# Performance work log

Hardware: AMD Instinct MI355X
Metric: run time of the kernel (lower is better)

The kernel has to match this reference:

```python
import jax, jax.numpy as jnp
import numpy as np

HEAD_NUM = 16

def setup_inputs() -> dict:
    key = jax.random.key(0)
    kq, kk, kv = jax.random.split(key, 3)
    shape = (4, 2048, 1024)  # [B, N, C]
    return {
        "query_layer": jax.random.normal(kq, shape, dtype=jnp.float32),
        "key_layer": jax.random.normal(kk, shape, dtype=jnp.float32),
        "value_layer": jax.random.normal(kv, shape, dtype=jnp.float32),
    }

def _split_heads(x, h):
    B, N, C = x.shape
    return x.reshape(B, N, h, C // h).transpose(0, 2, 1, 3)  # [B,H,N,d]

def reference(query_layer, key_layer, value_layer):
    B, N, C = query_layer.shape
    h = HEAD_NUM
    d = C // h
    q = _split_heads(query_layer, h)
    k = _split_heads(key_layer, h)
    v = _split_heads(value_layer, h)
    scores = jnp.einsum('bhnd,bhmd->bhnm', q, k) / jnp.sqrt(jnp.asarray(d, q.dtype))
    probs = jax.nn.softmax(scores, axis=-1)
    ctx = jnp.einsum('bhnm,bhmd->bhnd', probs, v)
    return ctx.transpose(0, 2, 1, 3).reshape(B, N, C)
```

## Files before the change

### kernel.cpp

```cpp
#include <hip/hip_runtime.h>
#include <hip/hip_bf16.h>

#define B_   4
#define N_   2048
#define C_   1024
#define NT   32
#define QSCALE 0.18033688011112042f

typedef __attribute__((ext_vector_type(8)))  short short8;
typedef __attribute__((ext_vector_type(4)))  float f32x4;
typedef __attribute__((ext_vector_type(16))) float f32x16;
typedef __attribute__((ext_vector_type(2)))  int   int2v;

__device__ __forceinline__ unsigned short f2bf(float x) {
    union { __hip_bfloat16 h; unsigned short u; } c;
    c.h = __float2bfloat16(x);
    return c.u;
}
__device__ __forceinline__ float fast_exp2(float x) {
    float r; asm("v_exp_f32 %0, %1" : "=v"(r) : "v"(x)); return r;
}
__device__ __forceinline__ int cvtpk(float a, float b) {
    int r; asm("v_cvt_pk_bf16_f32 %0, %1, %2" : "=v"(r) : "v"(a), "v"(b)); return r;
}

__global__ __launch_bounds__(256) void prepack(
    const float* __restrict__ K, const float* __restrict__ V,
    unsigned short* __restrict__ Kt, unsigned short* __restrict__ Vt)
{
    __shared__ __align__(16) unsigned short kl[4096];
    __shared__ __align__(16) unsigned short vl[4096];
    const int L = blockIdx.x;
    const int xcd = L & 7;
    const int j = L >> 3;
    const int head = xcd + 8 * (j >> 5);
    const int t = j & 31;
    const int b = head >> 4, h = head & 15;
    const int tid = threadIdx.x;
    const int r = tid >> 2, cb = tid & 3;
    const size_t head_off = (size_t)b * N_ * C_ + (size_t)h * 64;
    const int kv0 = t * 64;
    const int blk_out = head * NT + t;

    {
        const float* src = K + head_off + (size_t)(kv0 + r) * C_ + cb * 16;
        f32x4 x0 = *(const f32x4*)(src);
        f32x4 x1 = *(const f32x4*)(src + 4);
        f32x4 x2 = *(const f32x4*)(src + 8);
        f32x4 x3 = *(const f32x4*)(src + 12);
        short8 p0, p1;
        #pragma unroll
        for (int i = 0; i < 4; ++i) {
            p0[i] = (short)f2bf(x0[i]); p0[i + 4] = (short)f2bf(x1[i]);
            p1[i] = (short)f2bf(x2[i]); p1[i + 4] = (short)f2bf(x3[i]);
        }
        const int swz = (r & 7) << 3;
        *(short8*)&kl[r * 64 + ((cb * 16) ^ swz)]     = p0;
        *(short8*)&kl[r * 64 + ((cb * 16 + 8) ^ swz)] = p1;
    }
    {
        const float* src = V + head_off + (size_t)(kv0 + r) * C_ + cb * 16;
        f32x4 y0 = *(const f32x4*)(src);
        f32x4 y1 = *(const f32x4*)(src + 4);
        f32x4 y2 = *(const f32x4*)(src + 8);
        f32x4 y3 = *(const f32x4*)(src + 12);
        #pragma unroll
        for (int i = 0; i < 4; ++i) {
            int d0 = cb * 16 + i;
            vl[d0 * 64 + (r ^ ((d0 & 7) << 3))] = f2bf(y0[i]);
            int d1 = cb * 16 + 4 + i;
            vl[d1 * 64 + (r ^ ((d1 & 7) << 3))] = f2bf(y1[i]);
            int d2 = cb * 16 + 8 + i;
            vl[d2 * 64 + (r ^ ((d2 & 7) << 3))] = f2bf(y2[i]);
            int d3 = cb * 16 + 12 + i;
            vl[d3 * 64 + (r ^ ((d3 & 7) << 3))] = f2bf(y3[i]);
        }
    }
    __syncthreads();
    #pragma unroll
    for (int cc = 0; cc < 2; ++cc) {
        const int c  = tid + cc * 256;
        const int f  = c >> 6;
        const int ln = c & 63;
        const int row = (f & 1) * 32 + (ln & 31);
        const int col = (f >> 1) * 16 + (ln >> 5) * 8;
        const int sw  = (row & 7) << 3;
        short8 kk = *(const short8*)&kl[row * 64 + (col ^ sw)];
        short8 vv = *(const short8*)&vl[row * 64 + (col ^ sw)];
        *(short8*)&Kt[(size_t)blk_out * 4096 + c * 8] = kk;
        *(short8*)&Vt[(size_t)blk_out * 4096 + c * 8] = vv;
    }
}

#define MFMA32(A, B, C) __builtin_amdgcn_mfma_f32_32x32x16_bf16((A), (B), (C), 0, 0, 0)

#define TILE_BODY(T, PO0, PO1, PO2, PO3, PI0, PI1, PI2, PI3, FIRST)            \
{                                                                              \
    asm volatile("s_waitcnt vmcnt(0)" ::: "memory");                           \
    __syncthreads();                                                           \
    if ((T) + 1 < NT) stageK((T) + 1, cur ^ 1);                                \
    const unsigned short* kl = &klds[cur][0];                                  \
    f32x16 s0, s1;                                                             \
    {                                                                          \
        const float nm = (FIRST) ? 0.0f : -m_r;   \
        _Pragma("unroll")                                                      \
        for (int r = 0; r < 16; ++r) { s0[r] = nm; s1[r] = nm; }               \
    }                                                                          \
    __builtin_amdgcn_s_setprio(1);                                             \
    {                                                                          \
        short8 kf0 = *(const short8*)&kl[0 * 1024 + lofs];                     \
        short8 kf1 = *(const short8*)&kl[0 * 1024 + 512 + lofs];               \
        s0 = MFMA32(kf0, qfrag[0], s0);                                        \
        s1 = MFMA32(kf1, qfrag[0], s1);                                        \
        kf0 = *(const short8*)&kl[1 * 1024 + lofs];                            \
        kf1 = *(const short8*)&kl[1 * 1024 + 512 + lofs];                      \
        s0 = MFMA32(kf0, qfrag[1], s0);                                        \
        s1 = MFMA32(kf1, qfrag[1], s1);                                        \
        kf0 = *(const short8*)&kl[2 * 1024 + lofs];                            \
        kf1 = *(const short8*)&kl[2 * 1024 + 512 + lofs];                      \
        s0 = MFMA32(kf0, qfrag[2], s0);                                        \
        s1 = MFMA32(kf1, qfrag[2], s1);                                        \
        kf0 = *(const short8*)&kl[3 * 1024 + lofs];                            \
        kf1 = *(const short8*)&kl[3 * 1024 + 512 + lofs];                      \
        s0 = MFMA32(kf0, qfrag[3], s0);                                        \
        s1 = MFMA32(kf1, qfrag[3], s1);                                        \
    }                                                                          \
    if (!(FIRST)) {      \
        o0 = MFMA32(vr0, PI0, o0);  o1 = MFMA32(vr1, PI0, o1);                 \
        o0 = MFMA32(vr2, PI1, o0);  o1 = MFMA32(vr3, PI1, o1);                 \
        o0 = MFMA32(vr4, PI2, o0);  o1 = MFMA32(vr5, PI2, o1);                 \
        o0 = MFMA32(vr6, PI3, o0);  o1 = MFMA32(vr7, PI3, o1);                 \
    }                                                                          \
    __builtin_amdgcn_s_setprio(0);                                             \
    {                \
        const unsigned short* vtp = vbase + (size_t)(T) * 4096 + lofs;         \
        vr0 = *(const short8*)(vtp);                                           \
        vr1 = *(const short8*)(vtp + 512);                                     \
        vr2 = *(const short8*)(vtp + 1024);                                    \
        vr3 = *(const short8*)(vtp + 1536);                                    \
        vr4 = *(const short8*)(vtp + 2048);                                    \
        vr5 = *(const short8*)(vtp + 2560);                                    \
        vr6 = *(const short8*)(vtp + 3072);                                    \
        vr7 = *(const short8*)(vtp + 3584);                                    \
    }                                                                          \
    float mx[8];                                                               \
    _Pragma("unroll")                                                          \
    for (int r = 0; r < 8; ++r)                                                \
        mx[r] = fmaxf(fmaxf(s0[r], s0[r + 8]), fmaxf(s1[r], s1[r + 8]));       \
    _Pragma("unroll")                                                          \
    for (int st = 4; st; st >>= 1) {                                           \
        _Pragma("unroll")                                                      \
        for (int r = 0; r < st; ++r) mx[r] = fmaxf(mx[r], mx[r + st]);         \
    }                                                                          \
    int2v msw = __builtin_amdgcn_permlane32_swap(                              \
        __float_as_int(mx[0]), __float_as_int(mx[0]), false, false);           \
    const float rmp = fmaxf(__int_as_float(msw[0]), __int_as_float(msw[1]));   \
    if (FIRST) {                                                               \
        m_r = rmp;                                                             \
        _Pragma("unroll")                                                      \
        for (int r = 0; r < 16; ++r) { s0[r] -= rmp; s1[r] -= rmp; }           \
    } else if (!__all(rmp <= 8.0f)) {             \
        const float d = fmaxf(rmp, 0.0f);                                      \
        const float corr = fast_exp2(-d);                                      \
        m_r += d;                                                              \
        l_half *= corr;                                                        \
        _Pragma("unroll")                                                      \
        for (int r = 0; r < 16; ++r) {                                         \
            s0[r] -= d; s1[r] -= d;                                            \
            o0[r] *= corr; o1[r] *= corr;                                      \
        }                                                                      \
    }                                                                          \
    _Pragma("unroll")                                                          \
    for (int r = 0; r < 16; ++r) {                                             \
        s0[r] = fast_exp2(s0[r]);                                              \
        s1[r] = fast_exp2(s1[r]);                                              \
    }                                                                          \
    {                              \
        int w0, w1, w2, w3; int2v sA, sB;                                      \
        union { int i[4]; short8 v; } u;                                       \
        w0 = cvtpk(s0[0], s0[1]);  w1 = cvtpk(s0[2], s0[3]);                   \
        w2 = cvtpk(s0[4], s0[5]);  w3 = cvtpk(s0[6], s0[7]);                   \
        sA = __builtin_amdgcn_permlane32_swap(w0, w2, false, false);           \
        sB = __builtin_amdgcn_permlane32_swap(w1, w3, false, false);           \
        u.i[0] = sA[0]; u.i[1] = sB[0]; u.i[2] = sA[1]; u.i[3] = sB[1];        \
        PO0 = u.v;                                                             \
        w0 = cvtpk(s0[8], s0[9]);  w1 = cvtpk(s0[10], s0[11]);                 \
        w2 = cvtpk(s0[12], s0[13]); w3 = cvtpk(s0[14], s0[15]);                \
        sA = __builtin_amdgcn_permlane32_swap(w0, w2, false, false);           \
        sB = __builtin_amdgcn_permlane32_swap(w1, w3, false, false);           \
        u.i[0] = sA[0]; u.i[1] = sB[0]; u.i[2] = sA[1]; u.i[3] = sB[1];        \
        PO1 = u.v;                                                             \
        w0 = cvtpk(s1[0], s1[1]);  w1 = cvtpk(s1[2], s1[3]);                   \
        w2 = cvtpk(s1[4], s1[5]);  w3 = cvtpk(s1[6], s1[7]);                   \
        sA = __builtin_amdgcn_permlane32_swap(w0, w2, false, false);           \
        sB = __builtin_amdgcn_permlane32_swap(w1, w3, false, false);           \
        u.i[0] = sA[0]; u.i[1] = sB[0]; u.i[2] = sA[1]; u.i[3] = sB[1];        \
        PO2 = u.v;                                                             \
        w0 = cvtpk(s1[8], s1[9]);  w1 = cvtpk(s1[10], s1[11]);                 \
        w2 = cvtpk(s1[12], s1[13]); w3 = cvtpk(s1[14], s1[15]);                \
        sA = __builtin_amdgcn_permlane32_swap(w0, w2, false, false);           \
        sB = __builtin_amdgcn_permlane32_swap(w1, w3, false, false);           \
        u.i[0] = sA[0]; u.i[1] = sB[0]; u.i[2] = sA[1]; u.i[3] = sB[1];        \
        PO3 = u.v;                                                             \
    }                                                                          \
    float aa[8];                                                               \
    _Pragma("unroll")                                                          \
    for (int r = 0; r < 8; ++r) aa[r] = (s0[r] + s0[r + 8]) + (s1[r] + s1[r + 8]); \
    _Pragma("unroll")                                                          \
    for (int st = 4; st; st >>= 1) {                                           \
        _Pragma("unroll")                                                      \
        for (int r = 0; r < st; ++r) aa[r] += aa[r + st];                      \
    }                                                                          \
    l_half += aa[0];                                                           \
    cur ^= 1;                                                                  \
}

__global__ __launch_bounds__(256, 3) void attn_fwd(
    const float* __restrict__ Q, const unsigned short* __restrict__ Kt,
    const unsigned short* __restrict__ Vt, float* __restrict__ O)
{
    __shared__ __align__(16) unsigned short klds[2][4096];

    const int L = blockIdx.x;
    const int xcd = L & 7;
    const int j = L >> 3;
    const int head = xcd + 8 * (j >> 4);
    const int qt = j & 15;
    const int b = head >> 4, h = head & 15;

    const int tid  = threadIdx.x;
    const int wave = tid >> 6;
    const int lane = tid & 63;
    const int l31  = lane & 31;
    const int hi   = lane >> 5;

    const unsigned short* kbase = Kt + (size_t)head * (NT * 4096);
    const unsigned short* vbase = Vt + (size_t)head * (NT * 4096);
    const float* qp = Q + (size_t)b * N_ * C_ + (size_t)h * 64;
    float*       op = O + (size_t)b * N_ * C_ + (size_t)h * 64;

    const int qrow = qt * 128 + wave * 32 + l31;
    short8 qfrag[4];
    {
        const float* qr = qp + (size_t)qrow * C_ + hi * 8;
        #pragma unroll
        for (int ks = 0; ks < 4; ++ks) {
            f32x4 x0 = *(const f32x4*)(qr + ks * 16);
            f32x4 x1 = *(const f32x4*)(qr + ks * 16 + 4);
            short8 a;
            #pragma unroll
            for (int i = 0; i < 4; ++i) {
                a[i]     = (short)f2bf(x0[i] * QSCALE);
                a[i + 4] = (short)f2bf(x1[i] * QSCALE);
            }
            qfrag[ks] = a;
        }
    }

    f32x16 o0 = {}, o1 = {};
    float m_r = 0.0f, l_half = 0.0f;

    const int lofs = lane * 8;

    auto stageK = [&](int t, int buf) {
        const unsigned short* kg = kbase + (size_t)t * 4096 + wave * 1024 + lofs;
        __builtin_amdgcn_global_load_lds((const __attribute__((address_space(1))) void*)kg,
            (__attribute__((address_space(3))) void*)&klds[buf][wave * 1024], 16, 0, 0);
        __builtin_amdgcn_global_load_lds((const __attribute__((address_space(1))) void*)(kg + 512),
            (__attribute__((address_space(3))) void*)&klds[buf][wave * 1024 + 512], 16, 0, 0);
    };

    int cur = 0;
    short8 pA0, pA1, pA2, pA3, pB0, pB1, pB2, pB3;
    short8 vr0, vr1, vr2, vr3, vr4, vr5, vr6, vr7;

    stageK(0, 0);

    TILE_BODY(0, pA0, pA1, pA2, pA3, pB0, pB1, pB2, pB3, true)
    for (int t = 1; t < NT - 1; t += 2) {
        TILE_BODY(t,     pB0, pB1, pB2, pB3, pA0, pA1, pA2, pA3, false)
        TILE_BODY(t + 1, pA0, pA1, pA2, pA3, pB0, pB1, pB2, pB3, false)
    }
    TILE_BODY(NT - 1, pB0, pB1, pB2, pB3, pA0, pA1, pA2, pA3, false)

    __builtin_amdgcn_s_setprio(1);
    o0 = MFMA32(vr0, pB0, o0);  o1 = MFMA32(vr1, pB0, o1);
    o0 = MFMA32(vr2, pB1, o0);  o1 = MFMA32(vr3, pB1, o1);
    o0 = MFMA32(vr4, pB2, o0);  o1 = MFMA32(vr5, pB2, o1);
    o0 = MFMA32(vr6, pB3, o0);  o1 = MFMA32(vr7, pB3, o1);
    __builtin_amdgcn_s_setprio(0);

    int2v lsw = __builtin_amdgcn_permlane32_swap(
        __float_as_int(l_half), __float_as_int(l_half), false, false);
    const float l_r = __int_as_float(lsw[0]) + __int_as_float(lsw[1]);
    const float inv = 1.0f / l_r;

    float* orow = op + (size_t)qrow * C_;
    #pragma unroll
    for (int bb = 0; bb < 4; ++bb) {
        f32x4 w0, w1;
        #pragma unroll
        for (int i = 0; i < 4; ++i) {
            w0[i] = o0[4 * bb + i] * inv;
            w1[i] = o1[4 * bb + i] * inv;
        }
        *(f32x4*)(orow + 8 * bb + 4 * hi)      = w0;
        *(f32x4*)(orow + 32 + 8 * bb + 4 * hi) = w1;
    }
}

extern "C" void kernel_launch(void* const* d_in, const int* in_sizes, int n_in,
                              void* d_out, int out_size, void* d_ws, size_t ws_size,
                              hipStream_t stream) {
    const float* q = (const float*)d_in[0];
    const float* k = (const float*)d_in[1];
    const float* v = (const float*)d_in[2];
    float* o = (float*)d_out;
    unsigned short* Kt = (unsigned short*)d_ws;
    unsigned short* Vt = Kt + (size_t)64 * NT * 4096;
    prepack<<<dim3(64 * NT), dim3(256), 0, stream>>>(k, v, Kt, Vt);
    attn_fwd<<<dim3(1024), dim3(256), 0, stream>>>(q, Kt, Vt, o);
}
```

Before: 110.0 us.

## Software-pipeline QK of next tile with softmax of previous tile

Restructures the attention loop so the QK^T MFMAs for tile t run between the max/rescale and the exp/pack stages of tile t-1's softmax, using two ping-pong score buffers. The goal is to overlap MFMA work with the VALU exp and permute work. The barrier wait is relaxed to vmcnt(8) so the outstanding V register loads are not drained. The extra live score registers are paid for by lowering launch bounds from 3 to 2 waves per SIMD, which reduces occupancy.

```diff
diff --git a/kernel.cpp b/kernel.cpp
--- a/kernel.cpp
+++ b/kernel.cpp
@@ -94,59 +94,12 @@
 
 #define MFMA32(A, B, C) __builtin_amdgcn_mfma_f32_32x32x16_bf16((A), (B), (C), 0, 0, 0)
 
-#define TILE_BODY(T, PO0, PO1, PO2, PO3, PI0, PI1, PI2, PI3, FIRST)            \
-{                                                                              \
-    asm volatile("s_waitcnt vmcnt(0)" ::: "memory");                           \
-    __syncthreads();                                                           \
-    if ((T) + 1 < NT) stageK((T) + 1, cur ^ 1);                                \
-    const unsigned short* kl = &klds[cur][0];                                  \
-    f32x16 s0, s1;                                                             \
-    {                                                                          \
-        const float nm = (FIRST) ? 0.0f : -m_r;   \
-        _Pragma("unroll")                                                      \
-        for (int r = 0; r < 16; ++r) { s0[r] = nm; s1[r] = nm; }               \
-    }                                                                          \
-    __builtin_amdgcn_s_setprio(1);                                             \
-    {                                                                          \
-        short8 kf0 = *(const short8*)&kl[0 * 1024 + lofs];                     \
-        short8 kf1 = *(const short8*)&kl[0 * 1024 + 512 + lofs];               \
-        s0 = MFMA32(kf0, qfrag[0], s0);                                        \
-        s1 = MFMA32(kf1, qfrag[0], s1);                                        \
-        kf0 = *(const short8*)&kl[1 * 1024 + lofs];                            \
-        kf1 = *(const short8*)&kl[1 * 1024 + 512 + lofs];                      \
-        s0 = MFMA32(kf0, qfrag[1], s0);                                        \
-        s1 = MFMA32(kf1, qfrag[1], s1);                                        \
-        kf0 = *(const short8*)&kl[2 * 1024 + lofs];                            \
-        kf1 = *(const short8*)&kl[2 * 1024 + 512 + lofs];                      \
-        s0 = MFMA32(kf0, qfrag[2], s0);                                        \
-        s1 = MFMA32(kf1, qfrag[2], s1);                                        \
-        kf0 = *(const short8*)&kl[3 * 1024 + lofs];                            \
-        kf1 = *(const short8*)&kl[3 * 1024 + 512 + lofs];                      \
-        s0 = MFMA32(kf0, qfrag[3], s0);                                        \
-        s1 = MFMA32(kf1, qfrag[3], s1);                                        \
-    }                                                                          \
-    if (!(FIRST)) {      \
-        o0 = MFMA32(vr0, PI0, o0);  o1 = MFMA32(vr1, PI0, o1);                 \
-        o0 = MFMA32(vr2, PI1, o0);  o1 = MFMA32(vr3, PI1, o1);                 \
-        o0 = MFMA32(vr4, PI2, o0);  o1 = MFMA32(vr5, PI2, o1);                 \
-        o0 = MFMA32(vr6, PI3, o0);  o1 = MFMA32(vr7, PI3, o1);                 \
-    }                                                                          \
-    __builtin_amdgcn_s_setprio(0);                                             \
-    {                \
-        const unsigned short* vtp = vbase + (size_t)(T) * 4096 + lofs;         \
-        vr0 = *(const short8*)(vtp);                                           \
-        vr1 = *(const short8*)(vtp + 512);                                     \
-        vr2 = *(const short8*)(vtp + 1024);                                    \
-        vr3 = *(const short8*)(vtp + 1536);                                    \
-        vr4 = *(const short8*)(vtp + 2048);                                    \
-        vr5 = *(const short8*)(vtp + 2560);                                    \
-        vr6 = *(const short8*)(vtp + 3072);                                    \
-        vr7 = *(const short8*)(vtp + 3584);                                    \
-    }                                                                          \
+#define SM_HEAD(SB0, SB1, SMFIRST)                                             \
+{                                                                              \
     float mx[8];                                                               \
     _Pragma("unroll")                                                          \
     for (int r = 0; r < 8; ++r)                                                \
-        mx[r] = fmaxf(fmaxf(s0[r], s0[r + 8]), fmaxf(s1[r], s1[r + 8]));       \
+        mx[r] = fmaxf(fmaxf(SB0[r], SB0[r + 8]), fmaxf(SB1[r], SB1[r + 8]));   \
     _Pragma("unroll")                                                          \
     for (int st = 4; st; st >>= 1) {                                           \
         _Pragma("unroll")                                                      \
@@ -155,67 +108,129 @@
     int2v msw = __builtin_amdgcn_permlane32_swap(                              \
         __float_as_int(mx[0]), __float_as_int(mx[0]), false, false);           \
     const float rmp = fmaxf(__int_as_float(msw[0]), __int_as_float(msw[1]));   \
-    if (FIRST) {                                                               \
+    if (SMFIRST) {                                                             \
         m_r = rmp;                                                             \
         _Pragma("unroll")                                                      \
-        for (int r = 0; r < 16; ++r) { s0[r] -= rmp; s1[r] -= rmp; }           \
-    } else if (!__all(rmp <= 8.0f)) {             \
+        for (int r = 0; r < 16; ++r) { SB0[r] -= rmp; SB1[r] -= rmp; }         \
+    } else if (!__all(rmp <= 8.0f)) {                                          \
         const float d = fmaxf(rmp, 0.0f);                                      \
         const float corr = fast_exp2(-d);                                      \
         m_r += d;                                                              \
         l_half *= corr;                                                        \
         _Pragma("unroll")                                                      \
         for (int r = 0; r < 16; ++r) {                                         \
-            s0[r] -= d; s1[r] -= d;                                            \
+            SB0[r] -= d; SB1[r] -= d;                                          \
             o0[r] *= corr; o1[r] *= corr;                                      \
         }                                                                      \
     }                                                                          \
+}
+
+#define SM_TAIL(SB0, SB1)                                                      \
+{                                                                              \
     _Pragma("unroll")                                                          \
     for (int r = 0; r < 16; ++r) {                                             \
-        s0[r] = fast_exp2(s0[r]);                                              \
-        s1[r] = fast_exp2(s1[r]);                                              \
-    }                                                                          \
-    {                              \
+        SB0[r] = fast_exp2(SB0[r]);                                            \
+        SB1[r] = fast_exp2(SB1[r]);                                            \
+    }                                                                          \
+    {                                                                          \
         int w0, w1, w2, w3; int2v sA, sB;                                      \
         union { int i[4]; short8 v; } u;                                       \
-        w0 = cvtpk(s0[0], s0[1]);  w1 = cvtpk(s0[2], s0[3]);                   \
-        w2 = cvtpk(s0[4], s0[5]);  w3 = cvtpk(s0[6], s0[7]);                   \
+        w0 = cvtpk(SB0[0], SB0[1]);   w1 = cvtpk(SB0[2], SB0[3]);              \
+        w2 = cvtpk(SB0[4], SB0[5]);   w3 = cvtpk(SB0[6], SB0[7]);              \
         sA = __builtin_amdgcn_permlane32_swap(w0, w2, false, false);           \
         sB = __builtin_amdgcn_permlane32_swap(w1, w3, false, false);           \
         u.i[0] = sA[0]; u.i[1] = sB[0]; u.i[2] = sA[1]; u.i[3] = sB[1];        \
-        PO0 = u.v;                                                             \
-        w0 = cvtpk(s0[8], s0[9]);  w1 = cvtpk(s0[10], s0[11]);                 \
-        w2 = cvtpk(s0[12], s0[13]); w3 = cvtpk(s0[14], s0[15]);                \
+        pf0 = u.v;                                                             \
+        w0 = cvtpk(SB0[8], SB0[9]);   w1 = cvtpk(SB0[10], SB0[11]);            \
+        w2 = cvtpk(SB0[12], SB0[13]); w3 = cvtpk(SB0[14], SB0[15]);            \
         sA = __builtin_amdgcn_permlane32_swap(w0, w2, false, false);           \
         sB = __builtin_amdgcn_permlane32_swap(w1, w3, false, false);           \
         u.i[0] = sA[0]; u.i[1] = sB[0]; u.i[2] = sA[1]; u.i[3] = sB[1];        \
-        PO1 = u.v;                                                             \
-        w0 = cvtpk(s1[0], s1[1]);  w1 = cvtpk(s1[2], s1[3]);                   \
-        w2 = cvtpk(s1[4], s1[5]);  w3 = cvtpk(s1[6], s1[7]);                   \
+        pf1 = u.v;                                                             \
+        w0 = cvtpk(SB1[0], SB1[1]);   w1 = cvtpk(SB1[2], SB1[3]);              \
+        w2 = cvtpk(SB1[4], SB1[5]);   w3 = cvtpk(SB1[6], SB1[7]);              \
         sA = __builtin_amdgcn_permlane32_swap(w0, w2, false, false);           \
         sB = __builtin_amdgcn_permlane32_swap(w1, w3, false, false);           \
         u.i[0] = sA[0]; u.i[1] = sB[0]; u.i[2] = sA[1]; u.i[3] = sB[1];        \
-        PO2 = u.v;                                                             \
-        w0 = cvtpk(s1[8], s1[9]);  w1 = cvtpk(s1[10], s1[11]);                 \
-        w2 = cvtpk(s1[12], s1[13]); w3 = cvtpk(s1[14], s1[15]);                \
+        pf2 = u.v;                                                             \
+        w0 = cvtpk(SB1[8], SB1[9]);   w1 = cvtpk(SB1[10], SB1[11]);            \
+        w2 = cvtpk(SB1[12], SB1[13]); w3 = cvtpk(SB1[14], SB1[15]);            \
         sA = __builtin_amdgcn_permlane32_swap(w0, w2, false, false);           \
         sB = __builtin_amdgcn_permlane32_swap(w1, w3, false, false);           \
         u.i[0] = sA[0]; u.i[1] = sB[0]; u.i[2] = sA[1]; u.i[3] = sB[1];        \
-        PO3 = u.v;                                                             \
+        pf3 = u.v;                                                             \
     }                                                                          \
     float aa[8];                                                               \
     _Pragma("unroll")                                                          \
-    for (int r = 0; r < 8; ++r) aa[r] = (s0[r] + s0[r + 8]) + (s1[r] + s1[r + 8]); \
+    for (int r = 0; r < 8; ++r)                                                \
+        aa[r] = (SB0[r] + SB0[r + 8]) + (SB1[r] + SB1[r + 8]);                 \
     _Pragma("unroll")                                                          \
     for (int st = 4; st; st >>= 1) {                                           \
         _Pragma("unroll")                                                      \
         for (int r = 0; r < st; ++r) aa[r] += aa[r + st];                      \
     }                                                                          \
     l_half += aa[0];                                                           \
+}
+
+#define QK_SECTION(SA0, SA1)                                                   \
+{                                                                              \
+    const float nm = -m_r;                                                     \
+    _Pragma("unroll")                                                          \
+    for (int r = 0; r < 16; ++r) { SA0[r] = nm; SA1[r] = nm; }                 \
+    const unsigned short* kl = &klds[cur][0];                                  \
+    __builtin_amdgcn_s_setprio(1);                                             \
+    short8 kf0 = *(const short8*)&kl[0 * 1024 + lofs];                         \
+    short8 kf1 = *(const short8*)&kl[0 * 1024 + 512 + lofs];                   \
+    SA0 = MFMA32(kf0, qfrag[0], SA0);                                          \
+    SA1 = MFMA32(kf1, qfrag[0], SA1);                                          \
+    kf0 = *(const short8*)&kl[1 * 1024 + lofs];                                \
+    kf1 = *(const short8*)&kl[1 * 1024 + 512 + lofs];                          \
+    SA0 = MFMA32(kf0, qfrag[1], SA0);                                          \
+    SA1 = MFMA32(kf1, qfrag[1], SA1);                                          \
+    kf0 = *(const short8*)&kl[2 * 1024 + lofs];                                \
+    kf1 = *(const short8*)&kl[2 * 1024 + 512 + lofs];                          \
+    SA0 = MFMA32(kf0, qfrag[2], SA0);                                          \
+    SA1 = MFMA32(kf1, qfrag[2], SA1);                                          \
+    kf0 = *(const short8*)&kl[3 * 1024 + lofs];                                \
+    kf1 = *(const short8*)&kl[3 * 1024 + 512 + lofs];                          \
+    SA0 = MFMA32(kf0, qfrag[3], SA0);                                          \
+    SA1 = MFMA32(kf1, qfrag[3], SA1);                                          \
+    __builtin_amdgcn_s_setprio(0);                                             \
+}
+
+#define PV_SECTION()                                                           \
+{                                                                              \
+    __builtin_amdgcn_s_setprio(1);                                             \
+    o0 = MFMA32(vr0, pf0, o0);  o1 = MFMA32(vr1, pf0, o1);                     \
+    o0 = MFMA32(vr2, pf1, o0);  o1 = MFMA32(vr3, pf1, o1);                     \
+    o0 = MFMA32(vr4, pf2, o0);  o1 = MFMA32(vr5, pf2, o1);                     \
+    o0 = MFMA32(vr6, pf3, o0);  o1 = MFMA32(vr7, pf3, o1);                     \
+    __builtin_amdgcn_s_setprio(0);                                             \
+}
+
+#define V_LOAD(T)                                                              \
+{                                                                              \
+    const unsigned short* vtp = vbase + (size_t)(T) * 4096 + lofs;             \
+    vr0 = *(const short8*)(vtp);         vr1 = *(const short8*)(vtp + 512);    \
+    vr2 = *(const short8*)(vtp + 1024);  vr3 = *(const short8*)(vtp + 1536);   \
+    vr4 = *(const short8*)(vtp + 2048);  vr5 = *(const short8*)(vtp + 2560);   \
+    vr6 = *(const short8*)(vtp + 3072);  vr7 = *(const short8*)(vtp + 3584);   \
+}
+
+#define TILE_BODY2(T, SA0, SA1, SB0, SB1, SMFIRST)                             \
+{                                                                              \
+    asm volatile("s_waitcnt vmcnt(8) lgkmcnt(0)" ::: "memory");                \
+    __builtin_amdgcn_s_barrier();                                              \
+    if ((T) + 1 < NT) stageK((T) + 1, cur ^ 1);                                \
+    SM_HEAD(SB0, SB1, SMFIRST)                                                 \
+    QK_SECTION(SA0, SA1)                                                       \
+    SM_TAIL(SB0, SB1)                                                          \
+    PV_SECTION()                                                               \
+    V_LOAD(T)                                                                  \
     cur ^= 1;                                                                  \
 }
 
-__global__ __launch_bounds__(256, 3) void attn_fwd(
+__global__ __launch_bounds__(256, 2) void attn_fwd(
     const float* __restrict__ Q, const unsigned short* __restrict__ Kt,
     const unsigned short* __restrict__ Vt, float* __restrict__ O)
 {
@@ -258,6 +273,7 @@
     }
 
     f32x16 o0 = {}, o1 = {};
+    f32x16 sX0, sX1, sY0, sY1;
     float m_r = 0.0f, l_half = 0.0f;
 
     const int lofs = lane * 8;
@@ -271,24 +287,31 @@
     };
 
     int cur = 0;
-    short8 pA0, pA1, pA2, pA3, pB0, pB1, pB2, pB3;
+    short8 pf0, pf1, pf2, pf3;
     short8 vr0, vr1, vr2, vr3, vr4, vr5, vr6, vr7;
 
     stageK(0, 0);
-
-    TILE_BODY(0, pA0, pA1, pA2, pA3, pB0, pB1, pB2, pB3, true)
-    for (int t = 1; t < NT - 1; t += 2) {
-        TILE_BODY(t,     pB0, pB1, pB2, pB3, pA0, pA1, pA2, pA3, false)
-        TILE_BODY(t + 1, pA0, pA1, pA2, pA3, pB0, pB1, pB2, pB3, false)
-    }
-    TILE_BODY(NT - 1, pB0, pB1, pB2, pB3, pA0, pA1, pA2, pA3, false)
-
-    __builtin_amdgcn_s_setprio(1);
-    o0 = MFMA32(vr0, pB0, o0);  o1 = MFMA32(vr1, pB0, o1);
-    o0 = MFMA32(vr2, pB1, o0);  o1 = MFMA32(vr3, pB1, o1);
-    o0 = MFMA32(vr4, pB2, o0);  o1 = MFMA32(vr5, pB2, o1);
-    o0 = MFMA32(vr6, pB3, o0);  o1 = MFMA32(vr7, pB3, o1);
-    __builtin_amdgcn_s_setprio(0);
+    asm volatile("s_waitcnt vmcnt(0) lgkmcnt(0)" ::: "memory");
+    __syncthreads();
+
+    {
+        stageK(1, 1);
+        m_r = 0.0f;
+        QK_SECTION(sX0, sX1)
+        V_LOAD(0)
+        cur ^= 1;
+    }
+
+    TILE_BODY2(1, sY0, sY1, sX0, sX1, 1)
+
+    for (int t = 2; t < 31; t += 2) {
+        TILE_BODY2(t,     sX0, sX1, sY0, sY1, 0)
+        TILE_BODY2(t + 1, sY0, sY1, sX0, sX1, 0)
+    }
+
+    SM_HEAD(sY0, sY1, 0)
+    SM_TAIL(sY0, sY1)
+    PV_SECTION()
 
     int2v lsw = __builtin_amdgcn_permlane32_swap(
         __float_as_int(l_half), __float_as_int(l_half), false, false);
```

After: 211.3 us. 92.1% more time.
